# Kernel optimization log

Measured on AMD Instinct MI355X. Metric: run time of the kernel, lower is better.

## Reference

```python
import jax, jax.numpy as jnp
import numpy as np

HIDDEN = 64
SEQ_LEN = 128
BATCH = 64
T_MAX = 20.0
BW = 1.0


def setup_inputs() -> dict:
    key = jax.random.key(0)
    ks = jax.random.split(key, 8)
    s = 1.0 / np.sqrt(HIDDEN)
    return {
        "rand_uniform_pool": jax.random.uniform(ks[0], (BATCH, SEQ_LEN), jnp.float32, 1e-6, 1.0),
        "expert_time": jax.random.uniform(ks[1], (BATCH, SEQ_LEN), jnp.float32, 0.0, 1.0),
        "W_ih": jax.random.uniform(ks[2], (4 * HIDDEN, 1), jnp.float32, -s, s),
        "W_hh": jax.random.uniform(ks[3], (4 * HIDDEN, HIDDEN), jnp.float32, -s, s),
        "b_ih": jax.random.uniform(ks[4], (4 * HIDDEN,), jnp.float32, -s, s),
        "b_hh": jax.random.uniform(ks[5], (4 * HIDDEN,), jnp.float32, -s, s),
        "V_w": jax.random.uniform(ks[6], (1, HIDDEN), jnp.float32, -s, s),
        "V_b": jax.random.uniform(ks[7], (1,), jnp.float32, -s, s),
    }


def _generate_time(rand_uniform_pool, W_ih, W_hh, b_ih, b_hh, V_w, V_b):
    # sequential rollout over SEQ_LEN steps (data-dependent recurrence)
    u_seq = rand_uniform_pool.T[:, :, None]  # [S, B, 1]

    def step(carry, u):
        hx, cx, cum = carry
        sigma = jax.nn.elu(hx @ V_w.T + V_b) + 1.0            # [B, 1]
        cum = cum + (-jnp.log(u)) / sigma                      # exponential inter-event time
        gates = cum @ W_ih.T + b_ih + hx @ W_hh.T + b_hh       # [B, 4H]
        i, f, g, o = jnp.split(gates, 4, axis=1)               # torch LSTMCell gate order
        cx = jax.nn.sigmoid(f) * cx + jax.nn.sigmoid(i) * jnp.tanh(g)
        hx = jax.nn.sigmoid(o) * jnp.tanh(cx)
        return (hx, cx, cum), cum[:, 0]

    init = (jnp.zeros((BATCH, HIDDEN), jnp.float32),
            jnp.zeros((BATCH, HIDDEN), jnp.float32),
            jnp.zeros((BATCH, 1), jnp.float32))
    _, cums = jax.lax.scan(step, init, u_seq)                  # [S, B]
    return cums.T                                              # [B, S]


def _reward(expert_time, learner_time):
    N = BATCH * SEQ_LEN
    t_l = learner_time.reshape(N)
    t_e = expert_time.reshape(N)
    m_l = ((t_l < T_MAX) & (t_l > 0)).astype(jnp.float32)
    m_e = ((t_e < T_MAX) & (t_e > 0)).astype(jnp.float32)

    def ksum(a, b, ma, mb):
        # ma^T exp(-(a-b)^2/bw) mb without storing more than one NxN matrix at a time
        K = jnp.exp(-((b[:, None] - a[None, :]) ** 2) / BW)    # [N, N]
        return jnp.dot(mb, K @ ma)

    ee = ksum(t_e, t_e, m_e, m_e)
    ll = ksum(t_l, t_l, m_l, m_l)
    le = ksum(t_l, t_e, m_l, m_e)
    return (ee + ll - 2.0 * le).reshape(1, 1)


def reference(rand_uniform_pool, expert_time, W_ih, W_hh, b_ih, b_hh, V_w, V_b):
    learner_time = _generate_time(rand_uniform_pool, W_ih, W_hh, b_ih, b_hh, V_w, V_b)
    loss = _reward(expert_time, learner_time)
    return loss
```

## Files before the change

### kernel.cpp

```cpp
#include <hip/hip_runtime.h>
#include <math.h>

#define HIDDEN 64
#define SEQ 128
#define BATCH 64
#define NPTS (BATCH * SEQ)
#define TMAXV 20.0f
#define L2E 1.4426950408889634f
#define LN2 0.6931471805599453f

typedef float v2f __attribute__((ext_vector_type(2)));

__device__ __forceinline__ float fexp2(float x) { return __builtin_amdgcn_exp2f(x); }
__device__ __forceinline__ float flog2(float x) { return __builtin_amdgcn_logf(x); }
__device__ __forceinline__ float frcp(float x)  { return __builtin_amdgcn_rcpf(x); }
__device__ __forceinline__ float fsigmoid(float x) { return frcp(1.0f + fexp2(-x * L2E)); }
__device__ __forceinline__ float ftanh(float x)    { return 1.0f - 2.0f * frcp(1.0f + fexp2(2.0f * x * L2E)); }

template <int CTRL>
__device__ __forceinline__ float dpp_mov(float x) {
    int r = __builtin_amdgcn_update_dpp(0, __float_as_int(x), CTRL, 0xf, 0xf, false);
    return __int_as_float(r);
}
__device__ __forceinline__ float wave_sum_dpp(float x) {
    x += dpp_mov<0x111>(x);
    x += dpp_mov<0x112>(x);
    x += dpp_mov<0x114>(x);
    x += dpp_mov<0x118>(x);
    x += dpp_mov<0x142>(x);
    x += dpp_mov<0x143>(x);
    return __int_as_float(__builtin_amdgcn_readlane(__float_as_int(x), 63));
}

__device__ __forceinline__ float wave_sum_shfl(float v) {
    v += __shfl_xor(v, 1);  v += __shfl_xor(v, 2);  v += __shfl_xor(v, 4);
    v += __shfl_xor(v, 8);  v += __shfl_xor(v, 16); v += __shfl_xor(v, 32);
    return v;
}

__global__ __launch_bounds__(256) void gen_and_ee(
    const float* __restrict__ upool,
    const float* __restrict__ texp,
    const float* __restrict__ Wih,
    const float* __restrict__ Whh,
    const float* __restrict__ bih,
    const float* __restrict__ bhh,
    const float* __restrict__ Vw,
    const float* __restrict__ Vb,
    float* __restrict__ tl,
    float* __restrict__ out)
{
    __shared__ float lu_s[SEQ];
    __shared__ float act_s[2][256];
    __shared__ __align__(16) float hx_s[4][64];
    __shared__ float2 qbuf[2048];

    const int bid = blockIdx.x;
    const int tid = threadIdx.x;

    if (bid < BATCH) {
        const int h  = tid & 63;
        const int wv = tid >> 6;

        v2f w2[32];
        const float4* wrow = (const float4*)(Whh + tid * 64);
        #pragma unroll
        for (int k = 0; k < 16; ++k) {
            float4 v = wrow[k];
            w2[2 * k]     = (v2f){v.x, v.y};
            w2[2 * k + 1] = (v2f){v.z, v.w};
        }
        const float bias = bih[tid] + bhh[tid];
        const float wih  = Wih[tid];
        const float vw   = Vw[h];
        const float vb   = Vb[0];

        if (tid < SEQ) lu_s[tid] = -flog2(upool[bid * SEQ + tid]) * LN2;
        hx_s[wv][h] = 0.0f;
        float cx = 0.0f;
        __syncthreads();

        float sg0 = (vb > 0.0f) ? (vb + 1.0f) : fexp2(vb * L2E);
        float cum = lu_s[0] * frcp(sg0);
        if (tid == 0) tl[bid * SEQ + 0] = cum;

        for (int s = 0; s < SEQ - 1; ++s) {
            const float4* h4 = (const float4*)hx_s[wv];
            v2f a0 = {0.f, 0.f}, a1 = {0.f, 0.f}, a2 = {0.f, 0.f}, a3 = {0.f, 0.f};
            #pragma unroll
            for (int k = 0; k < 16; k += 2) {
                float4 va = h4[k];
                float4 vbq = h4[k + 1];
                a0 = a0 + w2[2 * k]     * (v2f){va.x, va.y};
                a1 = a1 + w2[2 * k + 1] * (v2f){va.z, va.w};
                a2 = a2 + w2[2 * k + 2] * (v2f){vbq.x, vbq.y};
                a3 = a3 + w2[2 * k + 3] * (v2f){vbq.z, vbq.w};
            }
            v2f aa = (a0 + a1) + (a2 + a3);
            float g = (aa.x + aa.y) + bias + cum * wih;
            float a = (wv == 2) ? ftanh(g) : fsigmoid(g);
            act_s[s & 1][tid] = a;
            __syncthreads();

            float ig = act_s[s & 1][h];
            float fg = act_s[s & 1][64 + h];
            float gg = act_s[s & 1][128 + h];
            float og = act_s[s & 1][192 + h];
            cx = fg * cx + ig * gg;
            float hx = og * ftanh(cx);
            hx_s[wv][h] = hx;

            float tot = wave_sum_dpp(hx * vw);
            float xx  = tot + vb;
            float sg  = (xx > 0.0f) ? (xx + 1.0f) : fexp2(xx * L2E);
            cum += lu_s[s + 1] * frcp(sg);
            if (tid == 0) tl[bid * SEQ + s + 1] = cum;
        }
    } else {
        const int eb = bid - BATCH;
        const int pc = eb & 31;
        const int qs = eb >> 5;

        const int p = pc * 256 + tid;
        const float tp = texp[p];
        const float mp = (tp < TMAXV && tp > 0.0f) ? 1.0f : 0.0f;

        const int q0 = qs * 2048;
        for (int i = tid; i < 2048; i += 256) {
            float tq = texp[q0 + i];
            float mq = (tq < TMAXV && tq > 0.0f) ? 1.0f : 0.0f;
            qbuf[i] = make_float2(tq, mq);
        }
        __syncthreads();

        float acc = 0.0f;
        #pragma unroll 4
        for (int i = 0; i < 2048; ++i) {
            float2 qq = qbuf[i];
            float d = tp - qq.x;
            acc = fmaf(qq.y, fexp2(d * d * (-L2E)), acc);
        }
        acc *= mp;
        acc = wave_sum_shfl(acc);
        if ((tid & 63) == 0) atomicAdd(out, acc);
    }
}

__global__ __launch_bounds__(256) void ll_le(
    const float* __restrict__ texp,
    const float* __restrict__ tl,
    float* __restrict__ out)
{
    __shared__ __align__(16) float4 qbuf[512];
    __shared__ float red[4];

    const int pc = blockIdx.x;
    const int qs = blockIdx.y;
    const int tid = threadIdx.x;

    const int p = pc * 256 + tid;
    const float tlp = tl[p];
    const float mlp = (tlp < TMAXV && tlp > 0.0f) ? 1.0f : 0.0f;

    const int q0 = qs * 512;
    for (int i = tid; i < 512; i += 256) {
        float tq = tl[q0 + i];
        float mq = (tq < TMAXV && tq > 0.0f) ? 1.0f : 0.0f;
        float te = texp[q0 + i];
        float me = (te < TMAXV && te > 0.0f) ? 1.0f : 0.0f;
        qbuf[i] = make_float4(tq, mq, te, me);
    }
    __syncthreads();

    float val = 0.0f;
    if (__ballot(mlp != 0.0f) != 0ULL) {
        float a_ll = 0.0f, a_le = 0.0f;
        #pragma unroll 4
        for (int i = 0; i < 512; ++i) {
            float4 q = qbuf[i];
            float d1 = tlp - q.x;
            a_ll = fmaf(q.y, fexp2(d1 * d1 * (-L2E)), a_ll);
            float d2 = tlp - q.z;
            a_le = fmaf(q.w, fexp2(d2 * d2 * (-L2E)), a_le);
        }
        val = mlp * (a_ll - 2.0f * a_le);
    }

    val = wave_sum_shfl(val);
    if ((tid & 63) == 0) red[tid >> 6] = val;
    __syncthreads();
    if (tid == 0) atomicAdd(out, red[0] + red[1] + red[2] + red[3]);
}

extern "C" void kernel_launch(void* const* d_in, const int* in_sizes, int n_in,
                              void* d_out, int out_size, void* d_ws, size_t ws_size,
                              hipStream_t stream) {
    const float* upool = (const float*)d_in[0];
    const float* texp  = (const float*)d_in[1];
    const float* Wih   = (const float*)d_in[2];
    const float* Whh   = (const float*)d_in[3];
    const float* bih   = (const float*)d_in[4];
    const float* bhh   = (const float*)d_in[5];
    const float* Vw    = (const float*)d_in[6];
    const float* Vb    = (const float*)d_in[7];
    float* out = (float*)d_out;
    float* tl  = (float*)d_ws;

    hipMemsetAsync(out, 0, sizeof(float), stream);
    hipLaunchKernelGGL(gen_and_ee, dim3(BATCH + 128), dim3(256), 0, stream,
                       upool, texp, Wih, Whh, bih, bhh, Vw, Vb, tl, out);
    hipLaunchKernelGGL(ll_le, dim3(32, 16), dim3(256), 0, stream, texp, tl, out);
}
```

Baseline: 160.9 us.

## Fuse LSTM rollout and kernel sums into one launch with compacted learner times

The recurrence now runs in a single wave per batch row. W_hh is held in registers as packed fp16 and the gate matvec uses fdot2 with readlane broadcasts, which removes the shared-memory and barrier traffic of each step. The separate ll/le kernel is merged into the same launch. Its blocks spin-wait on an atomic counter until all rollout waves finish, then work only over learner times below TMAX, which the rollout compacts via ballot and atomicAdd. This drops a launch and skips masked points, at the cost of fp16 precision in the recurrence, a spin-wait that deadlocks if the waiting blocks become resident before the producers, and a less parallel le/ll loop that reads global memory with no smem tiling.

```diff
diff --git a/kernel.cpp b/kernel.cpp
--- a/kernel.cpp
+++ b/kernel.cpp
@@ -1,213 +1,200 @@
 #include <hip/hip_runtime.h>
 #include <math.h>
 
-#define HIDDEN 64
-#define SEQ 128
-#define BATCH 64
-#define NPTS (BATCH * SEQ)
 #define TMAXV 20.0f
 #define L2E 1.4426950408889634f
 #define LN2 0.6931471805599453f
 
-typedef float v2f __attribute__((ext_vector_type(2)));
-
-__device__ __forceinline__ float fexp2(float x) { return __builtin_amdgcn_exp2f(x); }
-__device__ __forceinline__ float flog2(float x) { return __builtin_amdgcn_logf(x); }
-__device__ __forceinline__ float frcp(float x)  { return __builtin_amdgcn_rcpf(x); }
-__device__ __forceinline__ float fsigmoid(float x) { return frcp(1.0f + fexp2(-x * L2E)); }
-__device__ __forceinline__ float ftanh(float x)    { return 1.0f - 2.0f * frcp(1.0f + fexp2(2.0f * x * L2E)); }
+typedef __fp16 h2 __attribute__((ext_vector_type(2)));
+
+__device__ __forceinline__ float fexp2(float x){ return __builtin_amdgcn_exp2f(x); }
+__device__ __forceinline__ float flog2(float x){ return __builtin_amdgcn_logf(x); }
+__device__ __forceinline__ float frcp(float x){ return __builtin_amdgcn_rcpf(x); }
+__device__ __forceinline__ float fsig(float x){ return frcp(1.0f + fexp2(-x * L2E)); }
+__device__ __forceinline__ float ftanh_(float x){ return 1.0f - 2.0f * frcp(1.0f + fexp2(2.0f * x * L2E)); }
 
 template <int CTRL>
-__device__ __forceinline__ float dpp_mov(float x) {
-    int r = __builtin_amdgcn_update_dpp(0, __float_as_int(x), CTRL, 0xf, 0xf, false);
-    return __int_as_float(r);
-}
-__device__ __forceinline__ float wave_sum_dpp(float x) {
-    x += dpp_mov<0x111>(x);
-    x += dpp_mov<0x112>(x);
-    x += dpp_mov<0x114>(x);
-    x += dpp_mov<0x118>(x);
-    x += dpp_mov<0x142>(x);
-    x += dpp_mov<0x143>(x);
+__device__ __forceinline__ float dppmov(float x) {
+    return __int_as_float(__builtin_amdgcn_update_dpp(0, __float_as_int(x), CTRL, 0xf, 0xf, false));
+}
+__device__ __forceinline__ float wsum(float x) {
+    x += dppmov<0x111>(x);
+    x += dppmov<0x112>(x);
+    x += dppmov<0x114>(x);
+    x += dppmov<0x118>(x);
+    x += dppmov<0x142>(x);
+    x += dppmov<0x143>(x);
     return __int_as_float(__builtin_amdgcn_readlane(__float_as_int(x), 63));
 }
-
-__device__ __forceinline__ float wave_sum_shfl(float v) {
+__device__ __forceinline__ float wsum_shfl(float v) {
     v += __shfl_xor(v, 1);  v += __shfl_xor(v, 2);  v += __shfl_xor(v, 4);
     v += __shfl_xor(v, 8);  v += __shfl_xor(v, 16); v += __shfl_xor(v, 32);
     return v;
 }
 
-__global__ __launch_bounds__(256) void gen_and_ee(
-    const float* __restrict__ upool,
-    const float* __restrict__ texp,
+__global__ __launch_bounds__(256) void fused(
+    const float* __restrict__ up,
+    const float* __restrict__ te,
     const float* __restrict__ Wih,
     const float* __restrict__ Whh,
     const float* __restrict__ bih,
     const float* __restrict__ bhh,
     const float* __restrict__ Vw,
     const float* __restrict__ Vb,
-    float* __restrict__ tl,
+    unsigned int* __restrict__ hdr,
+    float* __restrict__ comp,
     float* __restrict__ out)
 {
-    __shared__ float lu_s[SEQ];
-    __shared__ float act_s[2][256];
-    __shared__ __align__(16) float hx_s[4][64];
     __shared__ float2 qbuf[2048];
-
     const int bid = blockIdx.x;
     const int tid = threadIdx.x;
 
-    if (bid < BATCH) {
-        const int h  = tid & 63;
-        const int wv = tid >> 6;
-
-        v2f w2[32];
-        const float4* wrow = (const float4*)(Whh + tid * 64);
+    if (bid < 64) {
+        if (tid >= 64) return;
+        const int l = tid;
+
+        h2 w[4][32];
         #pragma unroll
-        for (int k = 0; k < 16; ++k) {
-            float4 v = wrow[k];
-            w2[2 * k]     = (v2f){v.x, v.y};
-            w2[2 * k + 1] = (v2f){v.z, v.w};
-        }
-        const float bias = bih[tid] + bhh[tid];
-        const float wih  = Wih[tid];
-        const float vw   = Vw[h];
-        const float vb   = Vb[0];
-
-        if (tid < SEQ) lu_s[tid] = -flog2(upool[bid * SEQ + tid]) * LN2;
-        hx_s[wv][h] = 0.0f;
-        float cx = 0.0f;
-        __syncthreads();
+        for (int r = 0; r < 4; ++r) {
+            const float4* rp = (const float4*)(Whh + (r * 64 + l) * 64);
+            #pragma unroll
+            for (int j = 0; j < 16; ++j) {
+                float4 q = rp[j];
+                w[r][2 * j]     = __builtin_amdgcn_cvt_pkrtz(q.x, q.y);
+                w[r][2 * j + 1] = __builtin_amdgcn_cvt_pkrtz(q.z, q.w);
+            }
+        }
+        float bias[4], wih[4];
+        #pragma unroll
+        for (int r = 0; r < 4; ++r) {
+            bias[r] = bih[r * 64 + l] + bhh[r * 64 + l];
+            wih[r]  = Wih[r * 64 + l];
+        }
+        const float vwl = Vw[l];
+        const float vb  = Vb[0];
+        float lu0 = -flog2(up[bid * 128 + l]) * LN2;
+        float lu1 = -flog2(up[bid * 128 + 64 + l]) * LN2;
 
         float sg0 = (vb > 0.0f) ? (vb + 1.0f) : fexp2(vb * L2E);
-        float cum = lu_s[0] * frcp(sg0);
-        if (tid == 0) tl[bid * SEQ + 0] = cum;
-
-        for (int s = 0; s < SEQ - 1; ++s) {
-            const float4* h4 = (const float4*)hx_s[wv];
-            v2f a0 = {0.f, 0.f}, a1 = {0.f, 0.f}, a2 = {0.f, 0.f}, a3 = {0.f, 0.f};
+        float cum = __int_as_float(__builtin_amdgcn_readlane(__float_as_int(lu0), 0)) * frcp(sg0);
+        float h0 = (l == 0) ? cum : 1e30f;
+        float h1 = 1e30f;
+        float hx = 0.0f, cx = 0.0f;
+
+        for (int s = 0; s < 127; ++s) {
+            float hxn = dppmov<0xB1>(hx);
+            h2 hp = __builtin_amdgcn_cvt_pkrtz(hx, hxn);
+            int hpi = __builtin_bit_cast(int, hp);
+
+            float d0 = 0.f, d1 = 0.f, d2 = 0.f, d3 = 0.f;
             #pragma unroll
-            for (int k = 0; k < 16; k += 2) {
-                float4 va = h4[k];
-                float4 vbq = h4[k + 1];
-                a0 = a0 + w2[2 * k]     * (v2f){va.x, va.y};
-                a1 = a1 + w2[2 * k + 1] * (v2f){va.z, va.w};
-                a2 = a2 + w2[2 * k + 2] * (v2f){vbq.x, vbq.y};
-                a3 = a3 + w2[2 * k + 3] * (v2f){vbq.z, vbq.w};
-            }
-            v2f aa = (a0 + a1) + (a2 + a3);
-            float g = (aa.x + aa.y) + bias + cum * wih;
-            float a = (wv == 2) ? ftanh(g) : fsigmoid(g);
-            act_s[s & 1][tid] = a;
-            __syncthreads();
-
-            float ig = act_s[s & 1][h];
-            float fg = act_s[s & 1][64 + h];
-            float gg = act_s[s & 1][128 + h];
-            float og = act_s[s & 1][192 + h];
-            cx = fg * cx + ig * gg;
-            float hx = og * ftanh(cx);
-            hx_s[wv][h] = hx;
-
-            float tot = wave_sum_dpp(hx * vw);
+            for (int j = 0; j < 32; ++j) {
+                h2 b = __builtin_bit_cast(h2, __builtin_amdgcn_readlane(hpi, 2 * j));
+                d0 = __builtin_amdgcn_fdot2(w[0][j], b, d0, false);
+                d1 = __builtin_amdgcn_fdot2(w[1][j], b, d1, false);
+                d2 = __builtin_amdgcn_fdot2(w[2][j], b, d2, false);
+                d3 = __builtin_amdgcn_fdot2(w[3][j], b, d3, false);
+            }
+            float gi = fmaf(cum, wih[0], d0) + bias[0];
+            float gf = fmaf(cum, wih[1], d1) + bias[1];
+            float gg = fmaf(cum, wih[2], d2) + bias[2];
+            float go = fmaf(cum, wih[3], d3) + bias[3];
+            cx = fsig(gf) * cx + fsig(gi) * ftanh_(gg);
+            hx = fsig(go) * ftanh_(cx);
+
+            float tot = wsum(hx * vwl);
             float xx  = tot + vb;
             float sg  = (xx > 0.0f) ? (xx + 1.0f) : fexp2(xx * L2E);
-            cum += lu_s[s + 1] * frcp(sg);
-            if (tid == 0) tl[bid * SEQ + s + 1] = cum;
-        }
-    } else {
-        const int eb = bid - BATCH;
+            int idx = s + 1;
+            float lun = __int_as_float(__builtin_amdgcn_readlane(
+                            __float_as_int(idx < 64 ? lu0 : lu1), idx & 63));
+            cum += lun * frcp(sg);
+            h0 = (l == idx)      ? cum : h0;
+            h1 = (l == idx - 64) ? cum : h1;
+        }
+
+        unsigned long long b0 = __ballot(h0 < TMAXV);
+        unsigned long long b1 = __ballot(h1 < TMAXV);
+        int n0 = __popcll(b0), n1 = __popcll(b1);
+        int base = 0;
+        if (l == 0) base = (int)atomicAdd(&hdr[0], (unsigned)(n0 + n1));
+        base = __shfl(base, 0);
+        if (h0 < TMAXV) comp[base + l] = h0;
+        if (h1 < TMAXV) comp[base + 64 + l] = h1;
+        __threadfence();
+        if (l == 0) atomicAdd(&hdr[1], 1u);
+    } else if (bid < 192) {
+        const int eb = bid - 64;
         const int pc = eb & 31;
         const int qs = eb >> 5;
-
         const int p = pc * 256 + tid;
-        const float tp = texp[p];
+        const float tp = te[p];
         const float mp = (tp < TMAXV && tp > 0.0f) ? 1.0f : 0.0f;
-
         const int q0 = qs * 2048;
         for (int i = tid; i < 2048; i += 256) {
-            float tq = texp[q0 + i];
+            float tq = te[q0 + i];
             float mq = (tq < TMAXV && tq > 0.0f) ? 1.0f : 0.0f;
             qbuf[i] = make_float2(tq, mq);
         }
         __syncthreads();
-
         float acc = 0.0f;
         #pragma unroll 4
         for (int i = 0; i < 2048; ++i) {
-            float2 qq = qbuf[i];
-            float d = tp - qq.x;
-            acc = fmaf(qq.y, fexp2(d * d * (-L2E)), acc);
+            float2 q = qbuf[i];
+            float d = tp - q.x;
+            acc = fmaf(q.y, fexp2(d * d * (-L2E)), acc);
         }
         acc *= mp;
-        acc = wave_sum_shfl(acc);
+        acc = wsum_shfl(acc);
+        if ((tid & 63) == 0) atomicAdd(out, acc);
+    } else {
+        if (tid == 0) {
+            while (atomicAdd(&hdr[1], 0u) < 64u) __builtin_amdgcn_s_sleep(16);
+        }
+        __syncthreads();
+        __threadfence();
+        const int n = (int)*(volatile unsigned int*)&hdr[0];
+        const int gid = (bid - 192) * 256 + tid;
+        const int pg = gid >> 5;
+        const int sl = gid & 31;
+        float acc = 0.0f;
+        for (int pi = pg; pi < n; pi += 512) {
+            float tp = comp[pi];
+            float all_ = 0.0f, ale = 0.0f;
+            for (int j = sl; j < 8192; j += 32) {
+                float t = te[j];
+                float m = (t < TMAXV && t > 0.0f) ? 1.0f : 0.0f;
+                float d = tp - t;
+                ale = fmaf(m, fexp2(d * d * (-L2E)), ale);
+            }
+            for (int j = sl; j < n; j += 32) {
+                float d = tp - comp[j];
+                all_ += fexp2(d * d * (-L2E));
+            }
+            acc += all_ - 2.0f * ale;
+        }
+        acc = wsum_shfl(acc);
         if ((tid & 63) == 0) atomicAdd(out, acc);
     }
-}
-
-__global__ __launch_bounds__(256) void ll_le(
-    const float* __restrict__ texp,
-    const float* __restrict__ tl,
-    float* __restrict__ out)
-{
-    __shared__ __align__(16) float4 qbuf[512];
-    __shared__ float red[4];
-
-    const int pc = blockIdx.x;
-    const int qs = blockIdx.y;
-    const int tid = threadIdx.x;
-
-    const int p = pc * 256 + tid;
-    const float tlp = tl[p];
-    const float mlp = (tlp < TMAXV && tlp > 0.0f) ? 1.0f : 0.0f;
-
-    const int q0 = qs * 512;
-    for (int i = tid; i < 512; i += 256) {
-        float tq = tl[q0 + i];
-        float mq = (tq < TMAXV && tq > 0.0f) ? 1.0f : 0.0f;
-        float te = texp[q0 + i];
-        float me = (te < TMAXV && te > 0.0f) ? 1.0f : 0.0f;
-        qbuf[i] = make_float4(tq, mq, te, me);
-    }
-    __syncthreads();
-
-    float val = 0.0f;
-    if (__ballot(mlp != 0.0f) != 0ULL) {
-        float a_ll = 0.0f, a_le = 0.0f;
-        #pragma unroll 4
-        for (int i = 0; i < 512; ++i) {
-            float4 q = qbuf[i];
-            float d1 = tlp - q.x;
-            a_ll = fmaf(q.y, fexp2(d1 * d1 * (-L2E)), a_ll);
-            float d2 = tlp - q.z;
-            a_le = fmaf(q.w, fexp2(d2 * d2 * (-L2E)), a_le);
-        }
-        val = mlp * (a_ll - 2.0f * a_le);
-    }
-
-    val = wave_sum_shfl(val);
-    if ((tid & 63) == 0) red[tid >> 6] = val;
-    __syncthreads();
-    if (tid == 0) atomicAdd(out, red[0] + red[1] + red[2] + red[3]);
 }
 
 extern "C" void kernel_launch(void* const* d_in, const int* in_sizes, int n_in,
                               void* d_out, int out_size, void* d_ws, size_t ws_size,
                               hipStream_t stream) {
-    const float* upool = (const float*)d_in[0];
-    const float* texp  = (const float*)d_in[1];
-    const float* Wih   = (const float*)d_in[2];
-    const float* Whh   = (const float*)d_in[3];
-    const float* bih   = (const float*)d_in[4];
-    const float* bhh   = (const float*)d_in[5];
-    const float* Vw    = (const float*)d_in[6];
-    const float* Vb    = (const float*)d_in[7];
+    const float* up  = (const float*)d_in[0];
+    const float* te  = (const float*)d_in[1];
+    const float* Wih = (const float*)d_in[2];
+    const float* Whh = (const float*)d_in[3];
+    const float* bih = (const float*)d_in[4];
+    const float* bhh = (const float*)d_in[5];
+    const float* Vw  = (const float*)d_in[6];
+    const float* Vb  = (const float*)d_in[7];
+    unsigned int* hdr = (unsigned int*)d_ws;
+    float* comp = (float*)d_ws + 4;
     float* out = (float*)d_out;
-    float* tl  = (float*)d_ws;
-
-    hipMemsetAsync(out, 0, sizeof(float), stream);
-    hipLaunchKernelGGL(gen_and_ee, dim3(BATCH + 128), dim3(256), 0, stream,
-                       upool, texp, Wih, Whh, bih, bhh, Vw, Vb, tl, out);
-    hipLaunchKernelGGL(ll_le, dim3(32, 16), dim3(256), 0, stream, texp, tl, out);
-}
+
+    (void)hipMemsetAsync(d_ws, 0, 16, stream);
+    (void)hipMemsetAsync(d_out, 0, 4, stream);
+    hipLaunchKernelGGL(fused, dim3(256), dim3(256), 0, stream,
+                       up, te, Wih, Whh, bih, bhh, Vw, Vb, hdr, comp, out);
+}
```

After: 250.7 us. 1.56x slower.
